# Optimization experiments

Measured on AMD Instinct MI355X. Metric: run time of the kernel, lower is better.

Reference implementation:

```python
import jax, jax.numpy as jnp
import numpy as np

EPS = 1e-4
HEADS = 16
DH = 64


def setup_inputs() -> dict:
    key = jax.random.key(0)
    ks = jax.random.split(key, 5)
    b, t, d = 2, 2048, 1024
    return {
        "X": jax.random.normal(ks[0], (b, t, d), dtype=jnp.float32),
        "W_in": jax.random.normal(ks[1], (HEADS * 4 * DH, d), dtype=jnp.float32) * (1.0 / np.sqrt(d)),
        "b_in": jax.random.normal(ks[2], (HEADS * 4 * DH,), dtype=jnp.float32) * 0.01,
        "W_out": jax.random.normal(ks[3], (d, HEADS * DH), dtype=jnp.float32) * (1.0 / np.sqrt(HEADS * DH)),
        "b_out": jax.random.normal(ks[4], (d,), dtype=jnp.float32) * 0.01,
    }


def reference(X, W_in, b_in, W_out, b_out):
    b, t, d = X.shape
    # project_in: [b,t,h*4*dh] -> [b,t,h,4*dh] -> [b,h,t,4*dh]
    P = jnp.einsum('btd,ed->bte', X, W_in) + b_in
    P = P.reshape(b, t, HEADS, 4 * DH).transpose(0, 2, 1, 3)
    Q, K, V, G = jnp.split(P, 4, axis=-1)  # each [b,h,t,dh]
    # Euclidean cdist: sqrt(||q||^2 + ||k||^2 - 2 q.k), clamped at 0
    q2 = jnp.sum(Q * Q, axis=-1)[..., :, None]   # [b,h,t,1]
    k2 = jnp.sum(K * K, axis=-1)[..., None, :]   # [b,h,1,t]
    qk = jnp.einsum('bhqd,bhkd->bhqk', Q, K)
    dist = jnp.sqrt(jnp.maximum(q2 + k2 - 2.0 * qk, 0.0))
    # Shepard weights: (eps + dist)^-2, normalized over keys
    W = (EPS + dist) ** (-2)
    W = W / (EPS + jnp.sum(W, axis=-1, keepdims=True))
    A = jnp.einsum('bhqk,bhkd->bhqd', W, V)
    # gate, merge heads: [b,h,t,dh] -> [b,t,h*dh]
    H = (G * A).transpose(0, 2, 1, 3).reshape(b, t, HEADS * DH)
    Y = jnp.einsum('bte,de->btd', H, W_out) + b_out
    return Y
```

## Files before the change

### kernel.cpp

```cpp
#include <hip/hip_runtime.h>
#include <math.h>

#define EPS 1e-4f


typedef __attribute__((ext_vector_type(8))) short bf16x8;
typedef __attribute__((ext_vector_type(8))) unsigned short u16x8;
typedef __attribute__((ext_vector_type(4))) float f32x4;

#define MFMA(a, b, c) __builtin_amdgcn_mfma_f32_16x16x32_bf16(a, b, c, 0, 0, 0)

__device__ __forceinline__ unsigned short f2b(float f) {
    unsigned int u = __float_as_uint(f);
    u += 0x7fffu + ((u >> 16) & 1u);
    return (unsigned short)(u >> 16);
}
__device__ __forceinline__ float b2f(unsigned short u) {
    return __uint_as_float(((unsigned int)u) << 16);
}
__device__ __forceinline__ unsigned int cvtpk(float a, float b) {
    unsigned int r;
    asm("v_cvt_pk_bf16_f32 %0, %1, %2" : "=v"(r) : "v"(a), "v"(b));
    return r;
}

typedef __attribute__((address_space(1))) const unsigned int as1_u32;
typedef __attribute__((address_space(3))) unsigned int as3_u32;
__device__ __forceinline__ void gl_lds16(const unsigned short* g, unsigned short* l) {
    __builtin_amdgcn_global_load_lds((as1_u32*)g, (as3_u32*)l, 16, 0, 0);
}

__global__ __launch_bounds__(256)
void sga_f2b_all(const float* __restrict__ X, const float* __restrict__ Win,
                 const float* __restrict__ Wout,
                 unsigned short* __restrict__ Xb, unsigned short* __restrict__ Winb,
                 unsigned short* __restrict__ Woutb) {
    const int i = blockIdx.x * 256 + threadIdx.x;
    const float* src; unsigned short* dst; int off;
    if (i < 524288)        { src = X;    dst = Xb;    off = i; }
    else if (i < 1048576)  { src = Win;  dst = Winb;  off = i - 524288; }
    else                   { src = Wout; dst = Woutb; off = i - 1048576; }
    const float4* s = (const float4*)src + off * 2;
    float4 a = s[0], b = s[1];
    uint4 o;
    o.x = (unsigned)f2b(a.x) | ((unsigned)f2b(a.y) << 16);
    o.y = (unsigned)f2b(a.z) | ((unsigned)f2b(a.w) << 16);
    o.z = (unsigned)f2b(b.x) | ((unsigned)f2b(b.y) << 16);
    o.w = (unsigned)f2b(b.z) | ((unsigned)f2b(b.w) << 16);
    *((uint4*)dst + off) = o;
}

__global__ __launch_bounds__(256)
void sga_gemm1(const unsigned short* __restrict__ Xb, const unsigned short* __restrict__ Wb,
               const float* __restrict__ bin,
               unsigned short* __restrict__ Qb, unsigned short* __restrict__ Kb,
               unsigned short* __restrict__ Vt, unsigned short* __restrict__ Gb,
               float* __restrict__ q2s, float* __restrict__ k2s)
{
    __shared__ unsigned short As[128 * 64];
    __shared__ unsigned short Bs[128 * 64];
    const int tid = threadIdx.x;
    const int lane = tid & 63, w = tid >> 6;
    const int lr = lane & 15, lg = lane >> 4;
    const int wm = w & 1, wn = w >> 1;
    const int m0 = blockIdx.y * 128, n0 = blockIdx.x * 128;

    const int sr = tid >> 3, sc8 = tid & 7;
    const int gch = sc8 ^ (sr & 7);
    const unsigned short* aBase = Xb + (m0 + sr) * 1024 + gch * 8;
    const unsigned short* bBase = Wb + (n0 + sr) * 1024 + gch * 8;
    unsigned short* aDst = &As[w * 512];
    unsigned short* bDst = &Bs[w * 512];

    f32x4 acc[4][4] = {};

    for (int kt = 0; kt < 16; ++kt) {
        __syncthreads();
        #pragma unroll
        for (int c = 0; c < 4; ++c)
            gl_lds16(aBase + c * 32768 + kt * 64, aDst + c * 2048);
        #pragma unroll
        for (int c = 0; c < 4; ++c)
            gl_lds16(bBase + c * 32768 + kt * 64, bDst + c * 2048);
        __syncthreads();

        #pragma unroll
        for (int ks = 0; ks < 2; ++ks) {
            bf16x8 af[4], bfr[4];
            #pragma unroll
            for (int i = 0; i < 4; ++i) {
                const int row = wm * 64 + i * 16 + lr;
                af[i] = *(const bf16x8*)&As[row * 64 + (((ks * 4 + lg) ^ (row & 7)) * 8)];
            }
            #pragma unroll
            for (int i = 0; i < 4; ++i) {
                const int row = wn * 64 + i * 16 + lr;
                bfr[i] = *(const bf16x8*)&Bs[row * 64 + (((ks * 4 + lg) ^ (row & 7)) * 8)];
            }
            #pragma unroll
            for (int mi = 0; mi < 4; ++mi)
                #pragma unroll
                for (int ni = 0; ni < 4; ++ni)
                    acc[mi][ni] = MFMA(af[mi], bfr[ni], acc[mi][ni]);
        }
    }

    const int bb = m0 >> 11;
    const bool qkBlock = ((n0 & 128) == 0);
    #pragma unroll
    for (int mf = 0; mf < 4; ++mf) {
        const int tbase = m0 + wm * 64 + mf * 16 + lg * 4;
        const int tloc = tbase & 2047;
        float s2[4] = {0.f, 0.f, 0.f, 0.f};
        #pragma unroll
        for (int nf = 0; nf < 4; ++nf) {
            const int n = n0 + wn * 64 + nf * 16 + lr;
            const int h = n >> 8, cc = n & 255;
            const int part = cc >> 6, j = cc & 63;
            const int bh = bb * 16 + h;
            const float bz = bin[n];
            f32x4 v = acc[mf][nf];
            unsigned short e0 = f2b(v[0] + bz), e1 = f2b(v[1] + bz),
                           e2 = f2b(v[2] + bz), e3 = f2b(v[3] + bz);
            if (qkBlock) {
                float f0 = b2f(e0), f1 = b2f(e1), f2 = b2f(e2), f3 = b2f(e3);
                s2[0] += f0 * f0; s2[1] += f1 * f1;
                s2[2] += f2 * f2; s2[3] += f3 * f3;
            }
            if (part == 2) {
                ushort4 pk = make_ushort4(e0, e1, e2, e3);
                *(ushort4*)&Vt[(bh * 64 + j) * 2048 + tloc] = pk;
            } else {
                unsigned short* dst = (part == 0) ? Qb : ((part == 1) ? Kb : Gb);
                unsigned short vv[4] = {e0, e1, e2, e3};
                #pragma unroll
                for (int r = 0; r < 4; ++r)
                    dst[(bh * 2048 + tloc + r) * 64 + j] = vv[r];
            }
        }
        if (qkBlock) {
            const int bh = bb * 16 + (n0 >> 8);
            float* __restrict__ dstn = wn ? k2s : q2s;
            #pragma unroll
            for (int r = 0; r < 4; ++r) {
                float v = s2[r];
                v += __shfl_xor(v, 1, 64); v += __shfl_xor(v, 2, 64);
                v += __shfl_xor(v, 4, 64); v += __shfl_xor(v, 8, 64);
                if (lr == 0) dstn[bh * 2048 + ((tloc + r) & 2047)] = v;
            }
        }
    }
}

__global__ __launch_bounds__(256, 3)
void sga_attn(const unsigned short* __restrict__ Qb, const unsigned short* __restrict__ Kb,
              const unsigned short* __restrict__ Vt,
              const float* __restrict__ q2s, const float* __restrict__ k2s,
              unsigned short* __restrict__ Op0, unsigned short* __restrict__ Op1,
              unsigned short* __restrict__ Op2,
              float* __restrict__ Sw0, float* __restrict__ Sw1, float* __restrict__ Sw2)
{
    __shared__ unsigned short Klds[2 * 4096];
    __shared__ unsigned short Vlds[2 * 4096];
    __shared__ unsigned short Wlds[4 * 2048];

    const int tid = threadIdx.x;
    const int lane = tid & 63, w = tid >> 6;
    const int lr = lane & 15, lg = lane >> 4;

    const int lin = blockIdx.x;
    const int xcd = lin & 7, rem = lin >> 3;
    const int gid = xcd * 12 + (rem >> 4);
    const int qt = rem & 15;
    const int half = gid >> 5, bh = gid & 31;
    const int q0 = qt * 128 + w * 32;
    const int kbeg = half * 11;
    const int kend = (half == 2) ? 32 : (kbeg + 11);

    unsigned short* wl = &Wlds[w * 2048];
    unsigned short* __restrict__ Op = (half == 0) ? Op0 : ((half == 1) ? Op1 : Op2);
    float* __restrict__ Sw = (half == 0) ? Sw0 : ((half == 1) ? Sw1 : Sw2);

    const int srow = w * 16 + (lane >> 2);
    const int sc = (lane & 3) * 2;
    const unsigned short* Kg = Kb + (bh * 2048 + srow) * 64 + sc * 8;
    const unsigned short* Vg = Vt + (bh * 64 + srow) * 2048 + sc * 8;
    const int swz0 = srow * 64 + ((sc ^ (srow & 7)) * 8);
    const int swz1 = srow * 64 + (((sc + 1) ^ (srow & 7)) * 8);

    bf16x8 qf[2][2];
    #pragma unroll
    for (int g = 0; g < 2; ++g) {
        const unsigned short* qp = Qb + (bh * 2048 + q0 + g * 16 + lr) * 64 + lg * 8;
        qf[g][0] = *(const bf16x8*)qp;
        qf[g][1] = *(const bf16x8*)(qp + 32);
    }
    float q2v[2];
    q2v[0] = q2s[bh * 2048 + q0 + lr];
    q2v[1] = q2s[bh * 2048 + q0 + 16 + lr];

    f32x4 oacc[2][4] = {};
    float sumw[2] = {0.f, 0.f};

    uint4 ks0, ks1, vs0, vs1;
    {
        const unsigned short* kp = Kg + kbeg * 4096;
        ks0 = *(const uint4*)kp; ks1 = *(const uint4*)(kp + 8);
        const unsigned short* vp = Vg + kbeg * 64;
        vs0 = *(const uint4*)vp; vs1 = *(const uint4*)(vp + 8);
    }
    *(uint4*)&Klds[swz0] = ks0; *(uint4*)&Klds[swz1] = ks1;
    *(uint4*)&Vlds[swz0] = vs0; *(uint4*)&Vlds[swz1] = vs1;
    __syncthreads();

    int buf = 0;
    for (int kt = kbeg; kt < kend; ++kt) {
        const int k0 = kt * 64;
        const bool more = (kt + 1 < kend);

        if (more) {
            const unsigned short* kp = Kg + (kt + 1) * 4096;
            ks0 = *(const uint4*)kp; ks1 = *(const uint4*)(kp + 8);
            const unsigned short* vp = Vg + (kt + 1) * 64;
            vs0 = *(const uint4*)vp; vs1 = *(const uint4*)(vp + 8);
        }

        f32x4 k2v[4];
        #pragma unroll
        for (int nf = 0; nf < 4; ++nf)
            k2v[nf] = *(const f32x4*)&k2s[bh * 2048 + k0 + nf * 16 + lg * 4];

        f32x4 sa[2][4] = {};
        const unsigned short* kb = &Klds[buf * 4096];
        __builtin_amdgcn_s_setprio(1);
        #pragma unroll
        for (int nf = 0; nf < 4; ++nf) {
            const int row = nf * 16 + lr;
            bf16x8 kf0 = *(const bf16x8*)&kb[row * 64 + ((lg ^ (row & 7)) * 8)];
            bf16x8 kf1 = *(const bf16x8*)&kb[row * 64 + (((4 + lg) ^ (row & 7)) * 8)];
            #pragma unroll
            for (int g = 0; g < 2; ++g) {
                sa[g][nf] = MFMA(kf0, qf[g][0], sa[g][nf]);
                sa[g][nf] = MFMA(kf1, qf[g][1], sa[g][nf]);
            }
        }
        __builtin_amdgcn_s_setprio(0);

        #pragma unroll
        for (int g = 0; g < 2; ++g) {
            const int row = g * 16 + lr;
            #pragma unroll
            for (int nf = 0; nf < 4; ++nf) {
                float wv[4];
                #pragma unroll
                for (int r = 0; r < 4; ++r) {
                    float d2 = fmaf(-2.0f, sa[g][nf][r], q2v[g] + k2v[nf][r]);
                    d2 = fmaxf(d2, 1e-8f);
                    wv[r] = __builtin_amdgcn_rcpf(d2);
                    sumw[g] += wv[r];
                }
                uint2 pk;
                pk.x = cvtpk(wv[0], wv[1]);
                pk.y = cvtpk(wv[2], wv[3]);
                const int c = 2 * nf + (lg >> 1);
                *(uint2*)&wl[row * 64 + ((c ^ (row & 7)) * 8) + (lg & 1) * 4] = pk;
            }
        }

        bf16x8 pa[2][2];
        #pragma unroll
        for (int g = 0; g < 2; ++g) {
            const int row = g * 16 + lr;
            pa[g][0] = *(const bf16x8*)&wl[row * 64 + ((lg ^ (row & 7)) * 8)];
            pa[g][1] = *(const bf16x8*)&wl[row * 64 + (((4 + lg) ^ (row & 7)) * 8)];
        }
        const unsigned short* vb = &Vlds[buf * 4096];
        __builtin_amdgcn_s_setprio(1);
        #pragma unroll
        for (int vf = 0; vf < 4; ++vf) {
            const int row = vf * 16 + lr;
            bf16x8 v0 = *(const bf16x8*)&vb[row * 64 + ((lg ^ (row & 7)) * 8)];
            bf16x8 v1 = *(const bf16x8*)&vb[row * 64 + (((4 + lg) ^ (row & 7)) * 8)];
            #pragma unroll
            for (int g = 0; g < 2; ++g) {
                oacc[g][vf] = MFMA(pa[g][0], v0, oacc[g][vf]);
                oacc[g][vf] = MFMA(pa[g][1], v1, oacc[g][vf]);
            }
        }
        __builtin_amdgcn_s_setprio(0);

        if (more) {
            const int bo = (buf ^ 1) * 4096;
            *(uint4*)&Klds[bo + swz0] = ks0; *(uint4*)&Klds[bo + swz1] = ks1;
            *(uint4*)&Vlds[bo + swz0] = vs0; *(uint4*)&Vlds[bo + swz1] = vs1;
            __syncthreads();
            buf ^= 1;
        }
    }

    #pragma unroll
    for (int g = 0; g < 2; ++g) {
        sumw[g] += __shfl_xor(sumw[g], 16, 64);
        sumw[g] += __shfl_xor(sumw[g], 32, 64);
    }

    #pragma unroll
    for (int g = 0; g < 2; ++g) {
        #pragma unroll
        for (int vf = 0; vf < 4; ++vf) {
            #pragma unroll
            for (int r = 0; r < 4; ++r) {
                const int t = q0 + g * 16 + lg * 4 + r;
                const int dh = vf * 16 + lr;
                Op[(bh * 2048 + t) * 64 + dh] = f2b(oacc[g][vf][r]);
            }
        }
    }
    if (lg == 0) {
        Sw[bh * 2048 + q0 + lr]      = sumw[0];
        Sw[bh * 2048 + q0 + 16 + lr] = sumw[1];
    }
}

__global__ __launch_bounds__(256)
void sga_combine(const unsigned short* __restrict__ Op0, const unsigned short* __restrict__ Op1,
                 const unsigned short* __restrict__ Op2,
                 const float* __restrict__ Sw0, const float* __restrict__ Sw1,
                 const float* __restrict__ Sw2,
                 const unsigned short* __restrict__ Gb, unsigned short* __restrict__ Hb)
{
    const int idx = blockIdx.x * 256 + threadIdx.x;
    const int t16 = idx >> 3;
    const int dq = (idx & 7) << 3;
    u16x8 a = *(const u16x8*)&Op0[t16 * 64 + dq];
    u16x8 b = *(const u16x8*)&Op1[t16 * 64 + dq];
    u16x8 c = *(const u16x8*)&Op2[t16 * 64 + dq];
    u16x8 g = *(const u16x8*)&Gb[t16 * 64 + dq];
    const float s = Sw0[t16] + Sw1[t16] + Sw2[t16];
    const float inv = __builtin_amdgcn_rcpf(EPS + s);
    const int bh = t16 >> 11, tloc = t16 & 2047;
    const int bb = bh >> 4, h = bh & 15;
    u16x8 o;
    #pragma unroll
    for (int j = 0; j < 8; ++j)
        o[j] = f2b((b2f(a[j]) + b2f(b[j]) + b2f(c[j])) * inv * b2f(g[j]));
    *(u16x8*)&Hb[(bb * 2048 + tloc) * 1024 + h * 64 + dq] = o;
}

__global__ __launch_bounds__(256)
void sga_gemm2(const unsigned short* __restrict__ Hb, const unsigned short* __restrict__ Wb,
               const float* __restrict__ bout, float* __restrict__ Y)
{
    __shared__ unsigned short As[64 * 64];
    __shared__ unsigned short Bs[128 * 64];
    const int tid = threadIdx.x;
    const int lane = tid & 63, w = tid >> 6;
    const int lr = lane & 15, lg = lane >> 4;
    const int wm = w & 1, wn = w >> 1;
    const int m0 = blockIdx.y * 64, n0 = blockIdx.x * 128;

    const int sr = tid >> 3, sc8 = tid & 7;
    const int gch = sc8 ^ (sr & 7);
    const unsigned short* aBase = Hb + (m0 + sr) * 1024 + gch * 8;
    const unsigned short* bBase = Wb + (n0 + sr) * 1024 + gch * 8;
    unsigned short* aDst = &As[w * 512];
    unsigned short* bDst = &Bs[w * 512];

    f32x4 acc[2][4] = {};

    for (int kt = 0; kt < 16; ++kt) {
        __syncthreads();
        #pragma unroll
        for (int c = 0; c < 2; ++c)
            gl_lds16(aBase + c * 32768 + kt * 64, aDst + c * 2048);
        #pragma unroll
        for (int c = 0; c < 4; ++c)
            gl_lds16(bBase + c * 32768 + kt * 64, bDst + c * 2048);
        __syncthreads();

        #pragma unroll
        for (int ks = 0; ks < 2; ++ks) {
            bf16x8 af[2], bfr[4];
            #pragma unroll
            for (int i = 0; i < 2; ++i) {
                const int row = wm * 32 + i * 16 + lr;
                af[i] = *(const bf16x8*)&As[row * 64 + (((ks * 4 + lg) ^ (row & 7)) * 8)];
            }
            #pragma unroll
            for (int i = 0; i < 4; ++i) {
                const int row = wn * 64 + i * 16 + lr;
                bfr[i] = *(const bf16x8*)&Bs[row * 64 + (((ks * 4 + lg) ^ (row & 7)) * 8)];
            }
            #pragma unroll
            for (int mi = 0; mi < 2; ++mi)
                #pragma unroll
                for (int ni = 0; ni < 4; ++ni)
                    acc[mi][ni] = MFMA(af[mi], bfr[ni], acc[mi][ni]);
        }
    }

    #pragma unroll
    for (int mf = 0; mf < 2; ++mf) {
        const int m = m0 + wm * 32 + mf * 16 + lg * 4;
        #pragma unroll
        for (int nf = 0; nf < 4; ++nf) {
            const int n = n0 + wn * 64 + nf * 16 + lr;
            const float bz = bout[n];
            f32x4 v = acc[mf][nf];
            #pragma unroll
            for (int r = 0; r < 4; ++r)
                Y[(m + r) * 1024 + n] = v[r] + bz;
        }
    }
}

extern "C" void kernel_launch(void* const* d_in, const int* in_sizes, int n_in,
                              void* d_out, int out_size, void* d_ws, size_t ws_size,
                              hipStream_t stream) {
    const float* X    = (const float*)d_in[0];
    const float* Win  = (const float*)d_in[1];
    const float* bin  = (const float*)d_in[2];
    const float* Wout = (const float*)d_in[3];
    const float* bout = (const float*)d_in[4];
    float* Y = (float*)d_out;

    const int PER = 32 * 2048 * 64;
    unsigned short* Qb   = (unsigned short*)d_ws;
    unsigned short* Kb   = Qb + PER;
    unsigned short* Vt   = Kb + PER;
    unsigned short* Gb   = Vt + PER;
    unsigned short* Hb   = Gb + PER;
    unsigned short* Xb   = Hb + PER;
    unsigned short* Winb = Xb + PER;
    unsigned short* Woutb= Winb + PER;
    float* q2s = (float*)(Woutb + 1024 * 1024);
    float* k2s = q2s + 32 * 2048;
    float* Sw0 = k2s + 32 * 2048;
    float* Sw1 = Sw0 + 32 * 2048;
    float* Sw2 = Sw1 + 32 * 2048;
    unsigned short* Op2 = (unsigned short*)(Sw2 + 32 * 2048);
    unsigned short* Op0 = Xb;
    unsigned short* Op1 = Winb;

    sga_f2b_all<<<4608, 256, 0, stream>>>(X, Win, Wout, Xb, Winb, Woutb);
    sga_gemm1<<<dim3(32, 32), 256, 0, stream>>>(Xb, Winb, bin, Qb, Kb, Vt, Gb, q2s, k2s);
    sga_attn <<<1536, 256, 0, stream>>>(Qb, Kb, Vt, q2s, k2s, Op0, Op1, Op2, Sw0, Sw1, Sw2);
    sga_combine<<<2048, 256, 0, stream>>>(Op0, Op1, Op2, Sw0, Sw1, Sw2, Gb, Hb);
    sga_gemm2<<<dim3(8, 64), 256, 0, stream>>>(Hb, Woutb, bout, Y);
}
```

Before: 142.6 us.

## Keep Shepard weights in registers by permuting key rows to match MFMA layout

Remaps which key rows each MFMA fragment covers, so the QK accumulator output already has the register layout needed as the A operand of the PV MFMA. The per-wave LDS round-trip for the weight tile is removed. The K/V LDS swizzle is changed to fit the new row mapping, and occupancy is raised through launch bounds now that shared memory is smaller. The risks are register pressure from the higher occupancy target and bank conflicts under the new swizzle.

```diff
diff --git a/kernel.cpp b/kernel.cpp
--- a/kernel.cpp
+++ b/kernel.cpp
@@ -152,7 +152,7 @@
     }
 }
 
-__global__ __launch_bounds__(256, 3)
+__global__ __launch_bounds__(256, 5)
 void sga_attn(const unsigned short* __restrict__ Qb, const unsigned short* __restrict__ Kb,
               const unsigned short* __restrict__ Vt,
               const float* __restrict__ q2s, const float* __restrict__ k2s,
@@ -162,7 +162,6 @@
 {
     __shared__ unsigned short Klds[2 * 4096];
     __shared__ unsigned short Vlds[2 * 4096];
-    __shared__ unsigned short Wlds[4 * 2048];
 
     const int tid = threadIdx.x;
     const int lane = tid & 63, w = tid >> 6;
@@ -177,7 +176,6 @@
     const int kbeg = half * 11;
     const int kend = (half == 2) ? 32 : (kbeg + 11);
 
-    unsigned short* wl = &Wlds[w * 2048];
     unsigned short* __restrict__ Op = (half == 0) ? Op0 : ((half == 1) ? Op1 : Op2);
     float* __restrict__ Sw = (half == 0) ? Sw0 : ((half == 1) ? Sw1 : Sw2);
 
@@ -185,8 +183,12 @@
     const int sc = (lane & 3) * 2;
     const unsigned short* Kg = Kb + (bh * 2048 + srow) * 64 + sc * 8;
     const unsigned short* Vg = Vt + (bh * 64 + srow) * 2048 + sc * 8;
-    const int swz0 = srow * 64 + ((sc ^ (srow & 7)) * 8);
-    const int swz1 = srow * 64 + (((sc + 1) ^ (srow & 7)) * 8);
+    const int Ssw = (srow & 3) | (((srow >> 3) & 1) << 2);
+    const int swz0 = srow * 64 + ((sc ^ Ssw) * 8);
+    const int swz1 = srow * 64 + (((sc + 1) ^ Ssw) * 8);
+
+    const int Skr = (lr & 3) | (((lr >> 2) & 1) << 2);
+    const int Svr = (lr & 3) | (((lr >> 3) & 1) << 2);
 
     bf16x8 qf[2][2];
     #pragma unroll
@@ -227,17 +229,20 @@
 
         f32x4 k2v[4];
         #pragma unroll
-        for (int nf = 0; nf < 4; ++nf)
-            k2v[nf] = *(const f32x4*)&k2s[bh * 2048 + k0 + nf * 16 + lg * 4];
+        for (int nf = 0; nf < 4; ++nf) {
+            const int base_nf = ((nf & 1) << 2) + ((nf >> 1) << 5);
+            k2v[nf] = *(const f32x4*)&k2s[bh * 2048 + k0 + base_nf + lg * 8];
+        }
 
         f32x4 sa[2][4] = {};
         const unsigned short* kb = &Klds[buf * 4096];
         __builtin_amdgcn_s_setprio(1);
         #pragma unroll
         for (int nf = 0; nf < 4; ++nf) {
-            const int row = nf * 16 + lr;
-            bf16x8 kf0 = *(const bf16x8*)&kb[row * 64 + ((lg ^ (row & 7)) * 8)];
-            bf16x8 kf1 = *(const bf16x8*)&kb[row * 64 + (((4 + lg) ^ (row & 7)) * 8)];
+            const int arow = ((nf & 1) << 2) + ((nf >> 1) << 5)
+                           + ((lr >> 2) << 3) + (lr & 3);
+            bf16x8 kf0 = *(const bf16x8*)&kb[arow * 64 + ((lg ^ Skr) * 8)];
+            bf16x8 kf1 = *(const bf16x8*)&kb[arow * 64 + (((4 + lg) ^ Skr) * 8)];
             #pragma unroll
             for (int g = 0; g < 2; ++g) {
                 sa[g][nf] = MFMA(kf0, qf[g][0], sa[g][nf]);
@@ -246,41 +251,37 @@
         }
         __builtin_amdgcn_s_setprio(0);
 
+        bf16x8 pa[2][2];
         #pragma unroll
         for (int g = 0; g < 2; ++g) {
-            const int row = g * 16 + lr;
-            #pragma unroll
-            for (int nf = 0; nf < 4; ++nf) {
-                float wv[4];
+            #pragma unroll
+            for (int hf = 0; hf < 2; ++hf) {
+                uint4 t;
                 #pragma unroll
-                for (int r = 0; r < 4; ++r) {
-                    float d2 = fmaf(-2.0f, sa[g][nf][r], q2v[g] + k2v[nf][r]);
-                    d2 = fmaxf(d2, 1e-8f);
-                    wv[r] = __builtin_amdgcn_rcpf(d2);
-                    sumw[g] += wv[r];
+                for (int p = 0; p < 2; ++p) {
+                    const int nf = hf * 2 + p;
+                    float wv[4];
+                    #pragma unroll
+                    for (int r = 0; r < 4; ++r) {
+                        float d2 = fmaf(-2.0f, sa[g][nf][r], q2v[g] + k2v[nf][r]);
+                        d2 = fmaxf(d2, 1e-8f);
+                        wv[r] = __builtin_amdgcn_rcpf(d2);
+                        sumw[g] += wv[r];
+                    }
+                    if (p == 0) { t.x = cvtpk(wv[0], wv[1]); t.y = cvtpk(wv[2], wv[3]); }
+                    else        { t.z = cvtpk(wv[0], wv[1]); t.w = cvtpk(wv[2], wv[3]); }
                 }
-                uint2 pk;
-                pk.x = cvtpk(wv[0], wv[1]);
-                pk.y = cvtpk(wv[2], wv[3]);
-                const int c = 2 * nf + (lg >> 1);
-                *(uint2*)&wl[row * 64 + ((c ^ (row & 7)) * 8) + (lg & 1) * 4] = pk;
-            }
-        }
-
-        bf16x8 pa[2][2];
-        #pragma unroll
-        for (int g = 0; g < 2; ++g) {
-            const int row = g * 16 + lr;
-            pa[g][0] = *(const bf16x8*)&wl[row * 64 + ((lg ^ (row & 7)) * 8)];
-            pa[g][1] = *(const bf16x8*)&wl[row * 64 + (((4 + lg) ^ (row & 7)) * 8)];
-        }
+                pa[g][hf] = *(bf16x8*)&t;
+            }
+        }
+
         const unsigned short* vb = &Vlds[buf * 4096];
         __builtin_amdgcn_s_setprio(1);
         #pragma unroll
         for (int vf = 0; vf < 4; ++vf) {
             const int row = vf * 16 + lr;
-            bf16x8 v0 = *(const bf16x8*)&vb[row * 64 + ((lg ^ (row & 7)) * 8)];
-            bf16x8 v1 = *(const bf16x8*)&vb[row * 64 + (((4 + lg) ^ (row & 7)) * 8)];
+            bf16x8 v0 = *(const bf16x8*)&vb[row * 64 + ((lg ^ Svr) * 8)];
+            bf16x8 v1 = *(const bf16x8*)&vb[row * 64 + (((4 + lg) ^ Svr) * 8)];
             #pragma unroll
             for (int g = 0; g < 2; ++g) {
                 oacc[g][vf] = MFMA(pa[g][0], v0, oacc[g][vf]);
```

Result: slower. 334.3 us (+134.4%).
